# Kernel optimization log

Measured on AMD Instinct MI355X. Metric: run time of the kernel, lower is better.

The kernel has to match this reference:

```python
import jax, jax.numpy as jnp
import numpy as np

B, F, N, D, P = 32, 32, 36, 2048, 512  # batch, frames, objects, input dim, projected dim


def setup_inputs() -> dict:
    key = jax.random.key(0)
    ks = jax.random.split(key, 8)
    s = 1.0 / np.sqrt(D).astype(np.float32)  # torch nn.Linear default init range
    u = lambda k, shape: jax.random.uniform(k, shape, jnp.float32, -s, s)
    return {
        "object_variable": jax.random.normal(ks[0], (B, F, N, D), jnp.float32),
        "W_proj": u(ks[1], (D, P)), "b_proj": u(ks[2], (P,)),
        "W_sigma": u(ks[3], (D, P)), "b_sigma": u(ks[4], (P,)),
        "W_psi": u(ks[5], (D, P)), "b_psi": u(ks[6], (P,)),
        "W_r": u(ks[7], (D, P)),  # bias=False
    }


def reference(object_variable, W_proj, b_proj, W_sigma, b_sigma, W_psi, b_psi, W_r):
    # Dropouts are identity in eval mode.
    x = object_variable                                   # [B,F,N,D]
    r_feat = x @ W_proj + b_proj                          # [B,F,N,P]
    sig = x @ W_sigma + b_sigma                           # [B,F,N,P]
    psi = x @ W_psi + b_psi                               # [B,F,N,P]
    a_coeff = jnp.einsum('bfnp,bfmp->bfnm', sig, psi)     # [B,F,N,N] unscaled QK^T
    a_hat = jax.nn.softmax(a_coeff, axis=-1)
    r_hat = jnp.einsum('bfnm,bfmp->bfnp', a_hat, x @ W_r) # AV matmul
    return (r_feat, r_hat)
```

## Files before the change

kernel.cpp:

```cpp
#include <hip/hip_runtime.h>
#include <hip/hip_fp16.h>
#include <stdint.h>

typedef _Float16 half2v __attribute__((ext_vector_type(2)));
typedef _Float16 half4v __attribute__((ext_vector_type(4)));
typedef _Float16 half8v __attribute__((ext_vector_type(8)));
typedef float    float4v __attribute__((ext_vector_type(4)));

#define KDIM 2048
#define PDIM 512
#define MROWS 36864
#define NOBJ 36
#define NTOT 2048
#define KT   32

__device__ __forceinline__ void gload_lds16(const void* g, void* l) {
    using gptr_t = const __attribute__((address_space(1))) unsigned int*;
    using lptr_t = __attribute__((address_space(3))) unsigned int*;
    __builtin_amdgcn_global_load_lds((gptr_t)(uintptr_t)g,
                                     (lptr_t)(uint32_t)(uintptr_t)l,
                                     16, 0, 0);
}

__global__ __launch_bounds__(256)
void cvt_x_kernel(const float* __restrict__ x, _Float16* __restrict__ xh) {
    const size_t i = ((size_t)blockIdx.x * 256 + threadIdx.x) * 8;
    float4v a = *(const float4v*)&x[i];
    float4v b = *(const float4v*)&x[i + 4];
    half8v h;
    h[0] = (_Float16)a[0]; h[1] = (_Float16)a[1];
    h[2] = (_Float16)a[2]; h[3] = (_Float16)a[3];
    h[4] = (_Float16)b[0]; h[5] = (_Float16)b[1];
    h[6] = (_Float16)b[2]; h[7] = (_Float16)b[3];
    *(half8v*)&xh[i] = h;
}

__global__ __launch_bounds__(256)
void cvt_w_kernel(const float* __restrict__ Wp, const float* __restrict__ Ws,
                  const float* __restrict__ Wq, const float* __restrict__ Wr,
                  _Float16* __restrict__ wt) {
    const int bid = blockIdx.x;
    const int mat = bid >> 10;
    const int t   = bid & 1023;
    const int kt  = t >> 4;
    const int pt  = t & 15;
    const float* W = (mat == 0) ? Wp : (mat == 1) ? Ws : (mat == 2) ? Wq : Wr;

    __shared__ float tile[32][33];
    const int tx = threadIdx.x & 31;
    const int ty = threadIdx.x >> 5;
    #pragma unroll
    for (int r = 0; r < 4; ++r) {
        const int k = kt * 32 + ty + r * 8;
        tile[ty + r * 8][tx] = W[(size_t)k * PDIM + pt * 32 + tx];
    }
    __syncthreads();
    #pragma unroll
    for (int r = 0; r < 4; ++r) {
        const int p = pt * 32 + ty + r * 8;
        const int n = mat * PDIM + p;
        wt[(size_t)n * KDIM + kt * 32 + tx] = (_Float16)tile[tx][ty + r * 8];
    }
}

#define BARRIER() __builtin_amdgcn_s_barrier()

#define STAGE_AH(b_, kt_, h_) do {                                            \
    const _Float16* g_ = pA + (size_t)(kt_) * 64 + (size_t)(h_) * 262144;     \
    char* l_ = (char*)sA + (b_) * 32768 + (h_) * 16384 + tid * 16;            \
    gload_lds16(g_, l_);                                                      \
    gload_lds16(g_ + 131072, l_ + 8192);                                      \
} while (0)

#define STAGE_BH(b_, kt_, h_) do {                                            \
    const _Float16* g_ = pB + (size_t)(kt_) * 64 + (size_t)(h_) * 262144;     \
    char* l_ = (char*)sB + (b_) * 32768 + (h_) * 16384 + tid * 16;            \
    gload_lds16(g_, l_);                                                      \
    gload_lds16(g_ + 131072, l_ + 8192);                                      \
} while (0)

#define LOAD_AF(b_, qm_) do {                                                 \
    const char* ba_ = (const char*)sA + (b_) * 32768 + wrbase;                \
    _Pragma("unroll")                                                         \
    for (int mi = 0; mi < 4; ++mi) {                                          \
        const int ro_ = ((qm_) * 64 + mi * 16 + r15) * 128;                   \
        af[mi][0] = *(const half8v*)(ba_ + ro_ + ck0);                        \
        af[mi][1] = *(const half8v*)(ba_ + ro_ + ck1);                        \
    }                                                                         \
} while (0)

#define LOAD_BF(b_, qn_, dst_) do {                                           \
    const char* bb_ = (const char*)sB + (b_) * 32768 + wcbase;                \
    _Pragma("unroll")                                                         \
    for (int ni = 0; ni < 2; ++ni) {                                          \
        const int ro_ = (rB0 + (qn_) * 32 + ni * 16 + r15) * 128;             \
        dst_[ni][0] = *(const half8v*)(bb_ + ro_ + ck0);                      \
        dst_[ni][1] = *(const half8v*)(bb_ + ro_ + ck1);                      \
    }                                                                         \
} while (0)

#define MFMA16(mb_, nb_, bf_) do {                                            \
    _Pragma("unroll")                                                         \
    for (int mi = 0; mi < 4; ++mi)                                            \
        _Pragma("unroll")                                                     \
        for (int ni = 0; ni < 2; ++ni) {                                      \
            acc[(mb_) + mi][(nb_) + ni] = __builtin_amdgcn_mfma_f32_16x16x32_f16( \
                af[mi][0], bf_[ni][0], acc[(mb_) + mi][(nb_) + ni], 0, 0, 0); \
            acc[(mb_) + mi][(nb_) + ni] = __builtin_amdgcn_mfma_f32_16x16x32_f16( \
                af[mi][1], bf_[ni][1], acc[(mb_) + mi][(nb_) + ni], 0, 0, 0); \
        }                                                                     \
} while (0)

#define PHASE_SYNC() do {                                                     \
    BARRIER();                                                                \
    asm volatile("s_waitcnt lgkmcnt(0)" ::: "memory");                        \
    __builtin_amdgcn_sched_barrier(0);                                        \
} while (0)

#define ITER(t_, b_) do {                                                     \
                                                        \
    LOAD_AF(b_, 0); LOAD_BF(b_, 0, b0);                                       \
    if ((t_) + 1 < KT) STAGE_AH((b_) ^ 1, (t_) + 1, 0);                       \
    PHASE_SYNC();                                                             \
    __builtin_amdgcn_s_setprio(1); MFMA16(0, 0, b0);                          \
    __builtin_amdgcn_s_setprio(0); BARRIER();                                 \
                                                        \
    LOAD_BF(b_, 1, b1);                                                       \
    if ((t_) + 1 < KT) STAGE_AH((b_) ^ 1, (t_) + 1, 1);                       \
    PHASE_SYNC();                                                             \
    __builtin_amdgcn_s_setprio(1); MFMA16(0, 2, b1);                          \
    __builtin_amdgcn_s_setprio(0); BARRIER();                                 \
                                                        \
    LOAD_AF(b_, 1);                                                           \
    if ((t_) + 2 < KT) STAGE_BH(b_, (t_) + 2, 0);                             \
    PHASE_SYNC();                                                             \
    __builtin_amdgcn_s_setprio(1); MFMA16(4, 2, b1);                          \
    __builtin_amdgcn_s_setprio(0); BARRIER();                                 \
                      \
    if ((t_) + 2 < KT) STAGE_BH(b_, (t_) + 2, 1);                             \
    __builtin_amdgcn_s_setprio(1); MFMA16(4, 0, b0);                          \
    __builtin_amdgcn_s_setprio(0);                                            \
    if ((t_) + 2 < KT)      { asm volatile("s_waitcnt vmcnt(4)" ::: "memory"); } \
    else if ((t_) + 1 < KT) { asm volatile("s_waitcnt vmcnt(0)" ::: "memory"); } \
    BARRIER();                                                                \
} while (0)

__global__ __launch_bounds__(512, 2)
void proj_gemm(const _Float16* __restrict__ A, const _Float16* __restrict__ Bt,
               float* __restrict__ rfeat, _Float16* __restrict__ sg,
               _Float16* __restrict__ ph, _Float16* __restrict__ vh,
               const float* __restrict__ bp, const float* __restrict__ bs,
               const float* __restrict__ bq) {
    __shared__ _Float16 sA[2][2][8192];
    __shared__ _Float16 sB[2][2][8192];

    const int tid  = threadIdx.x;
    const int lane = tid & 63;
    const int wid  = tid >> 6;
    const int wr   = wid >> 2;
    const int wc   = wid & 3;
    const int r15  = lane & 15;
    const int k4   = lane >> 4;

    const int bid = blockIdx.x;
    const int swz = (bid & 7) * 144 + (bid >> 3);
    const int mt  = swz >> 3, nt = swz & 7;
    const int m0  = mt * 256, n0 = nt * 256;

    const int srow = tid >> 3;
    const int sk   = (tid & 7) ^ (srow & 7);
    const _Float16* pA = A  + (size_t)(m0 + srow) * KDIM + sk * 8;
    const _Float16* pB = Bt + (size_t)(n0 + srow) * KDIM + sk * 8;

    const int ck0 = ((k4)     ^ (r15 & 7)) * 16;
    const int ck1 = ((4 + k4) ^ (r15 & 7)) * 16;
    const int wrbase = wr * 16384;
    const int wcbase = (wc >> 1) * 16384;
    const int rB0    = (wc & 1) * 64;

    half8v af[4][2], b0[2][2], b1[2][2];
    float4v acc[8][4] = {};

    STAGE_AH(0, 0, 0); STAGE_AH(0, 0, 1);
    STAGE_BH(0, 0, 0); STAGE_BH(0, 0, 1);
    STAGE_BH(1, 1, 0); STAGE_BH(1, 1, 1);
    asm volatile("s_waitcnt vmcnt(4)" ::: "memory");
    BARRIER();

    for (int tt = 0; tt < KT; tt += 2) {
        ITER(tt, 0);
        ITER(tt + 1, 1);
    }

    const int seg = n0 >> 9;
    const int pn0 = (n0 & 511) + wc * 64;
    #pragma unroll
    for (int ni = 0; ni < 4; ++ni) {
        const int pcol = pn0 + ni * 16 + r15;
        float bias = 0.0f;
        if (seg == 0)      bias = bp[pcol];
        else if (seg == 1) bias = bs[pcol];
        else if (seg == 2) bias = bq[pcol];
        #pragma unroll
        for (int mi = 0; mi < 8; ++mi) {
            const int rb = m0 + wr * 128 + mi * 16 + k4 * 4;
            #pragma unroll
            for (int r = 0; r < 4; ++r) {
                const float val = acc[mi][ni][r] + bias;
                const size_t off = (size_t)(rb + r) * PDIM + pcol;
                if (seg == 0)      rfeat[off] = val;
                else if (seg == 1) sg[off] = (_Float16)val;
                else if (seg == 2) ph[off] = (_Float16)val;
                else               vh[off] = (_Float16)val;
            }
        }
    }
}

__global__ __launch_bounds__(256, 2)
void attn_kernel(const _Float16* __restrict__ sg, const _Float16* __restrict__ ph,
                 const _Float16* __restrict__ vh, float* __restrict__ rhat) {
    __shared__ _Float16 ss[NOBJ * 520];
    __shared__ _Float16 ps[NOBJ * 520];
    __shared__ float    Ls[NOBJ * 37];

    const int tid = threadIdx.x;
    const size_t base = (size_t)blockIdx.x * (NOBJ * PDIM);

    for (int c = tid; c < (NOBJ * PDIM / 8); c += 256) {
        const int row = c >> 6;
        const int col = (c & 63) * 8;
        *(half8v*)&ss[row * 520 + col] = *(const half8v*)&sg[base + row * PDIM + col];
        *(half8v*)&ps[row * 520 + col] = *(const half8v*)&ph[base + row * PDIM + col];
    }
    __syncthreads();

    if (tid < 144) {
        const int i0 = (tid / 12) * 3;
        const int j0 = (tid % 12) * 3;
        float accv[3][3] = {};
        for (int p = 0; p < PDIM; p += 8) {
            half8v si[3], pj[3];
            #pragma unroll
            for (int ii = 0; ii < 3; ++ii) si[ii] = *(const half8v*)&ss[(i0 + ii) * 520 + p];
            #pragma unroll
            for (int jj = 0; jj < 3; ++jj) pj[jj] = *(const half8v*)&ps[(j0 + jj) * 520 + p];
            #pragma unroll
            for (int ii = 0; ii < 3; ++ii)
                #pragma unroll
                for (int jj = 0; jj < 3; ++jj) {
                    float t = accv[ii][jj];
                    #pragma unroll
                    for (int q = 0; q < 4; ++q) {
                        half2v x2; x2[0] = si[ii][2 * q]; x2[1] = si[ii][2 * q + 1];
                        half2v y2; y2[0] = pj[jj][2 * q]; y2[1] = pj[jj][2 * q + 1];
                        t = __builtin_amdgcn_fdot2(x2, y2, t, false);
                    }
                    accv[ii][jj] = t;
                }
        }
        #pragma unroll
        for (int ii = 0; ii < 3; ++ii)
            #pragma unroll
            for (int jj = 0; jj < 3; ++jj)
                Ls[(i0 + ii) * 37 + (j0 + jj)] = accv[ii][jj];
    }
    __syncthreads();

    if (tid < NOBJ) {
        float mx = -1e30f;
        for (int j = 0; j < NOBJ; ++j) mx = fmaxf(mx, Ls[tid * 37 + j]);
        float sum = 0.0f;
        for (int j = 0; j < NOBJ; ++j) {
            float e = __expf(Ls[tid * 37 + j] - mx);
            sum += e;
            Ls[tid * 37 + j] = e;
        }
        const float inv = 1.0f / sum;
        for (int j = 0; j < NOBJ; ++j) Ls[tid * 37 + j] *= inv;
    }
    __syncthreads();

    const int p4 = (tid & 127) * 4;
    const int r0 = tid >> 7;
    float4v acc[18] = {};
    for (int j = 0; j < NOBJ; ++j) {
        half4v v4 = *(const half4v*)&vh[base + (size_t)j * PDIM + p4];
        float4v vf;
        vf[0] = (float)v4[0]; vf[1] = (float)v4[1];
        vf[2] = (float)v4[2]; vf[3] = (float)v4[3];
        #pragma unroll
        for (int m = 0; m < 18; ++m) {
            const float aw = Ls[(2 * m + r0) * 37 + j];
            acc[m] += aw * vf;
        }
    }
    #pragma unroll
    for (int m = 0; m < 18; ++m)
        *(float4v*)&rhat[base + (size_t)(2 * m + r0) * PDIM + p4] = acc[m];
}

extern "C" void kernel_launch(void* const* d_in, const int* in_sizes, int n_in,
                              void* d_out, int out_size, void* d_ws, size_t ws_size,
                              hipStream_t stream) {
    const float* x   = (const float*)d_in[0];
    const float* Wp  = (const float*)d_in[1];
    const float* bp  = (const float*)d_in[2];
    const float* Wsg = (const float*)d_in[3];
    const float* bsg = (const float*)d_in[4];
    const float* Wps = (const float*)d_in[5];
    const float* bps = (const float*)d_in[6];
    const float* Wr  = (const float*)d_in[7];
    float* out = (float*)d_out;

    char* ws = (char*)d_ws;
    _Float16* xh = (_Float16*)(ws);
    _Float16* wt = (_Float16*)(ws + 150994944UL);
    _Float16* sg = (_Float16*)(ws + 159383552UL);
    _Float16* ph = (_Float16*)(ws + 197132288UL);
    _Float16* vh = (_Float16*)(ws + 234881024UL);

    cvt_x_kernel<<<36864, 256, 0, stream>>>(x, xh);
    cvt_w_kernel<<<4096, 256, 0, stream>>>(Wp, Wsg, Wps, Wr, wt);
    proj_gemm<<<144 * 8, 512, 0, stream>>>(xh, wt, out, sg, ph, vh, bp, bsg, bps);
    attn_kernel<<<1024, 256, 0, stream>>>(sg, ph, vh, out + 18874368);
}
```

Measured before the change: 851.9 us.

## Collapse four-phase GEMM main loop into two phases with fewer barriers

Restructures the projection GEMM's per-tile iteration from four barrier-separated phases into two. All next-tile A staging is issued up front, then all B fragments and the first A fragment are read from LDS, followed by the first half of the MFMAs. After a single barrier, the next-next B tile is staged and the second half of the MFMAs runs. This removes several workgroup barriers and explicit lgkmcnt waits per K-step. In exchange, LDS reads overlap less finely with MFMA work, more fragments are live in registers at once, and more global-to-LDS traffic is issued in bursts.

```diff
diff --git a/kernel.cpp b/kernel.cpp
--- a/kernel.cpp
+++ b/kernel.cpp
@@ -111,34 +111,20 @@
         }                                                                     \
 } while (0)
 
-#define PHASE_SYNC() do {                                                     \
+#define ITER(t_, b_) do {                                                     \
+    if ((t_) + 1 < KT) { STAGE_AH((b_) ^ 1, (t_) + 1, 0);                     \
+                         STAGE_AH((b_) ^ 1, (t_) + 1, 1); }                   \
+    LOAD_BF(b_, 0, b0); LOAD_BF(b_, 1, b1); LOAD_AF(b_, 0);                   \
+    __builtin_amdgcn_s_setprio(1);                                            \
+    MFMA16(0, 0, b0); MFMA16(0, 2, b1);                                       \
+    __builtin_amdgcn_s_setprio(0);                                            \
+    __builtin_amdgcn_sched_barrier(0);     \
     BARRIER();                                                                \
-    asm volatile("s_waitcnt lgkmcnt(0)" ::: "memory");                        \
-    __builtin_amdgcn_sched_barrier(0);                                        \
-} while (0)
-
-#define ITER(t_, b_) do {                                                     \
-                                                        \
-    LOAD_AF(b_, 0); LOAD_BF(b_, 0, b0);                                       \
-    if ((t_) + 1 < KT) STAGE_AH((b_) ^ 1, (t_) + 1, 0);                       \
-    PHASE_SYNC();                                                             \
-    __builtin_amdgcn_s_setprio(1); MFMA16(0, 0, b0);                          \
-    __builtin_amdgcn_s_setprio(0); BARRIER();                                 \
-                                                        \
-    LOAD_BF(b_, 1, b1);                                                       \
-    if ((t_) + 1 < KT) STAGE_AH((b_) ^ 1, (t_) + 1, 1);                       \
-    PHASE_SYNC();                                                             \
-    __builtin_amdgcn_s_setprio(1); MFMA16(0, 2, b1);                          \
-    __builtin_amdgcn_s_setprio(0); BARRIER();                                 \
-                                                        \
+    if ((t_) + 2 < KT) { STAGE_BH(b_, (t_) + 2, 0);                           \
+                         STAGE_BH(b_, (t_) + 2, 1); }                         \
     LOAD_AF(b_, 1);                                                           \
-    if ((t_) + 2 < KT) STAGE_BH(b_, (t_) + 2, 0);                             \
-    PHASE_SYNC();                                                             \
-    __builtin_amdgcn_s_setprio(1); MFMA16(4, 2, b1);                          \
-    __builtin_amdgcn_s_setprio(0); BARRIER();                                 \
-                      \
-    if ((t_) + 2 < KT) STAGE_BH(b_, (t_) + 2, 1);                             \
-    __builtin_amdgcn_s_setprio(1); MFMA16(4, 0, b0);                          \
+    __builtin_amdgcn_s_setprio(1);                                            \
+    MFMA16(4, 0, b0); MFMA16(4, 2, b1);                                       \
     __builtin_amdgcn_s_setprio(0);                                            \
     if ((t_) + 2 < KT)      { asm volatile("s_waitcnt vmcnt(4)" ::: "memory"); } \
     else if ((t_) + 1 < KT) { asm volatile("s_waitcnt vmcnt(0)" ::: "memory"); } \
```

New measurement: 847.3 us. Within noise of the previous version (-0.5%).
